# Optimization experiments

Measured on AMD Instinct MI355X. Metric: run time of the kernel, lower is better.

The kernel has to match this reference:

```python
import jax, jax.numpy as jnp
import numpy as np

STATE_LEN = 128
SEQ_LEN = 2048
NUM_ITERS = 2
DIM_IN = 1024
DIM_H = 64
BATCH = 2
T_TOTAL = SEQ_LEN + 2 * STATE_LEN  # 2304
NEG = -1e30  # large-negative causal mask (avoids -inf NaNs under autodiff)


def _ln(x, g, b):
    m = jnp.mean(x, axis=-1, keepdims=True)
    v = jnp.var(x, axis=-1, keepdims=True)
    return (x - m) / jnp.sqrt(v + 1e-5) * g + b


def setup_inputs() -> dict:
    key = jax.random.key(0)
    ks = jax.random.split(key, 16)

    def w(k, fi, fo):
        # torch nn.Linear-style fan-in scaled init (keeps logits O(1))
        return jax.random.normal(k, (fi, fo), jnp.float32) / np.sqrt(fi)

    return {
        "x": jax.random.normal(ks[0], (BATCH, T_TOTAL, DIM_IN), jnp.float32),
        "Wh": w(ks[1], DIM_IN, DIM_H),
        "Whs": w(ks[2], DIM_IN, DIM_H),
        "Whe": w(ks[3], DIM_IN, DIM_H),
        "Wk": w(ks[4], DIM_H, DIM_H),
        "Wq": w(ks[5], DIM_H, DIM_H),
        "Wv": w(ks[6], DIM_H, DIM_H),
        "Wks": w(ks[7], DIM_H, DIM_H),
        "Wqs": w(ks[8], DIM_H, DIM_H),
        "Wvs": w(ks[9], DIM_H, DIM_H),
        "Wke": w(ks[10], DIM_H, DIM_H),
        "Wqe": w(ks[11], DIM_H, DIM_H),
        "Wve": w(ks[12], DIM_H, DIM_H),
        "ln_g": jnp.ones((DIM_IN,), jnp.float32),
        "ln_b": jnp.zeros((DIM_IN,), jnp.float32),
        "ln_gs": jnp.ones((DIM_IN,), jnp.float32),
        "ln_bs": jnp.zeros((DIM_IN,), jnp.float32),
        "ln_ge": jnp.ones((DIM_IN,), jnp.float32),
        "ln_be": jnp.zeros((DIM_IN,), jnp.float32),
        "cope_emb": jax.random.normal(ks[13], (DIM_H, T_TOTAL), jnp.float32),
    }


def reference(x, Wh, Whs, Whe, Wk, Wq, Wv, Wks, Wqs, Wvs, Wke, Wqe, Wve,
              ln_g, ln_b, ln_gs, ln_bs, ln_ge, ln_be, cope_emb):
    S = STATE_LEN
    # extract_state: [state_start | seq | state_end] along token dim
    xs, xm, xe = x[:, :S], x[:, S:-S], x[:, -S:]
    xm = _ln(xm, ln_g, ln_b)
    xs = _ln(xs, ln_gs, ln_bs)
    xe = _ln(xe, ln_ge, ln_be)

    mem = xm @ Wh                 # (B, L, D)
    mem_s = xs @ Whs              # (B, S, D)
    mem_e = xe @ Whe              # (B, S, D)

    scale = 1.0 / np.sqrt(DIM_H)  # xformers default scale (beta=None)
    tril = jnp.tril(jnp.ones((T_TOTAL, T_TOTAL), bool))
    mask = jnp.where(tril, 0.0, NEG)  # log of lower-triangular ones

    mem_full = None
    for ix in range(NUM_ITERS):
        k = jnp.concatenate([mem_s @ Wks, mem @ Wk, mem_e @ Wke], axis=1)  # (B,T,D)
        q = jnp.concatenate([mem_s @ Wqs, mem @ Wq, mem_e @ Wqe], axis=1)
        v = jnp.concatenate([mem_s @ Wvs, mem @ Wv, mem_e @ Wve], axis=1)

        logits = jnp.einsum('btd,bsd->bts', q, k)  # unscaled, as in CoPE gates
        if ix == 0:
            # CoPE: sigmoid-gated reverse cumsum positions + interpolated embedding bias
            gates = jax.nn.sigmoid(logits)
            pos = jnp.flip(jnp.cumsum(jnp.flip(gates, -1), axis=-1), -1)
            pos = jnp.minimum(pos, float(T_TOTAL - 1))
            pos_floor = jnp.floor(pos)
            pos_ceil = jnp.ceil(pos)
            logits_int = jnp.einsum('btd,dn->btn', q, cope_emb)  # (B,T,T)
            lc = jnp.take_along_axis(logits_int, pos_ceil.astype(jnp.int32), axis=-1)
            lf = jnp.take_along_axis(logits_int, pos_floor.astype(jnp.int32), axis=-1)
            wfrac = pos - pos_floor
            bias = lc * wfrac + lf * (1.0 - wfrac)
            scores = logits * scale + mask + bias
        else:
            scores = logits * scale + mask

        attn = jax.nn.softmax(scores, axis=-1)
        mem_full = jnp.einsum('bts,bsd->btd', attn, v)  # (B,T,D)
        if ix < NUM_ITERS - 1:
            mem_s, mem, mem_e = mem_full[:, :S], mem_full[:, S:-S], mem_full[:, -S:]
    return mem_full
```

## Files before the change

### kernel.cpp

```cpp
#include <hip/hip_runtime.h>

#define T_TOT 2304
#define S_LEN 128
#define D_IN  1024
#define D_H   64
#define BATCH 2
#define NROW  (BATCH * T_TOT)
#define CH    (T_TOT / 256)
#define SCALE 0.125f
#define KCHUNKS 8
#define KCW   (D_IN / KCHUNKS)
#define TB    16
#define FCH   288
#define NSC   8
#define NTBLK (T_TOT / TB)

typedef unsigned short u16;
typedef __attribute__((ext_vector_type(8))) short short8;
typedef __attribute__((ext_vector_type(4))) float f32x4;
typedef __attribute__((ext_vector_type(4))) unsigned short u16x4;

static __device__ __forceinline__ u16 f2bf(float f) {
    unsigned u = __float_as_uint(f);
    unsigned r = (u + 0x7fffu + ((u >> 16) & 1u)) >> 16;
    return (u16)r;
}
static __device__ __forceinline__ float bf2f(u16 s) {
    return __uint_as_float((unsigned)s << 16);
}

__global__ __launch_bounds__(256) void k_ln(
    const float* __restrict__ x,
    const float* __restrict__ ln_g,  const float* __restrict__ ln_b,
    const float* __restrict__ ln_gs, const float* __restrict__ ln_bs,
    const float* __restrict__ ln_ge, const float* __restrict__ ln_be,
    u16* __restrict__ xn_hi, u16* __restrict__ xn_lo)
{
    __shared__ float red1[256], red2[256];
    const int row = blockIdx.x;
    const int t = row % T_TOT;
    const int tid = threadIdx.x;

    const float *gg, *bb;
    if (t < S_LEN)               { gg = ln_gs; bb = ln_bs; }
    else if (t >= T_TOT - S_LEN) { gg = ln_ge; bb = ln_be; }
    else                         { gg = ln_g;  bb = ln_b;  }

    const float4 xv = *(const float4*)(x + (size_t)row * D_IN + 4 * tid);
    float s  = xv.x + xv.y + xv.z + xv.w;
    float s2 = xv.x * xv.x + xv.y * xv.y + xv.z * xv.z + xv.w * xv.w;
    red1[tid] = s; red2[tid] = s2; __syncthreads();
    for (int off = 128; off > 0; off >>= 1) {
        if (tid < off) { red1[tid] += red1[tid + off]; red2[tid] += red2[tid + off]; }
        __syncthreads();
    }
    const float mean = red1[0] * (1.f / D_IN);
    const float var  = red2[0] * (1.f / D_IN) - mean * mean;
    const float rstd = rsqrtf(var + 1e-5f);

    const float4 gv = *(const float4*)(gg + 4 * tid);
    const float4 bv = *(const float4*)(bb + 4 * tid);
    float o0 = (xv.x - mean) * rstd * gv.x + bv.x;
    float o1 = (xv.y - mean) * rstd * gv.y + bv.y;
    float o2 = (xv.z - mean) * rstd * gv.z + bv.z;
    float o3 = (xv.w - mean) * rstd * gv.w + bv.w;

    u16x4 hv, lv;
    hv[0] = f2bf(o0); lv[0] = f2bf(o0 - bf2f(hv[0]));
    hv[1] = f2bf(o1); lv[1] = f2bf(o1 - bf2f(hv[1]));
    hv[2] = f2bf(o2); lv[2] = f2bf(o2 - bf2f(hv[2]));
    hv[3] = f2bf(o3); lv[3] = f2bf(o3 - bf2f(hv[3]));
    *(u16x4*)(xn_hi + (size_t)row * D_IN + 4 * tid) = hv;
    *(u16x4*)(xn_lo + (size_t)row * D_IN + 4 * tid) = lv;
}

#define WPREP_N (3 * D_H * D_IN)
__global__ __launch_bounds__(256) void k_prep(
    const float* __restrict__ Wh, const float* __restrict__ Whs, const float* __restrict__ Whe,
    const float* __restrict__ cope,
    u16* __restrict__ wT_hi, u16* __restrict__ wT_lo,
    u16* __restrict__ cT_hi, u16* __restrict__ cT_lo)
{
    const int gid = blockIdx.x * 256 + threadIdx.x;
    if (gid < WPREP_N) {
        const int seg = gid >> 16;
        const int o = gid & 65535;
        const int j = o >> 10, k = o & 1023;
        const float* W = seg == 0 ? Wh : (seg == 1 ? Whs : Whe);
        const float f = W[k * D_H + j];
        const u16 hi = f2bf(f);
        wT_hi[gid] = hi;
        wT_lo[gid] = f2bf(f - bf2f(hi));
    } else {
        const int idx = gid - WPREP_N;
        if (idx < T_TOT * D_H) {
            const int n = idx >> 6, d = idx & 63;
            const float f = cope[(size_t)d * T_TOT + n];
            const u16 hi = f2bf(f);
            cT_hi[idx] = hi;
            cT_lo[idx] = f2bf(f - bf2f(hi));
        }
    }
}

__global__ __launch_bounds__(256) void k_hgemm(
    const u16* __restrict__ xn_hi, const u16* __restrict__ xn_lo,
    const u16* __restrict__ wT_hi, const u16* __restrict__ wT_lo,
    float* __restrict__ h_part)
{
    const int tile = blockIdx.x;
    const int kc   = blockIdx.y;
    const int k0   = kc * KCW;
    const int tt = tile % 36;
    const int seg = tt < 2 ? 1 : (tt >= 34 ? 2 : 0);

    __shared__ u16 Bh[64 * KCW];
    __shared__ u16 Bl[64 * KCW];

    const int tid = threadIdx.x;
    {
        const int r = tid >> 2;
        const int c0 = (tid & 3) * 32;
        const u16* sh = wT_hi + ((size_t)seg * D_H + r) * D_IN + k0 + c0;
        const u16* sl = wT_lo + ((size_t)seg * D_H + r) * D_IN + k0 + c0;
        const int sw = (r & 7) << 3;
        #pragma unroll
        for (int u = 0; u < 4; ++u) {
            const int col = c0 + 8 * u;
            *(short8*)&Bh[r * KCW + (col ^ sw)] = *(const short8*)(sh + 8 * u);
            *(short8*)&Bl[r * KCW + (col ^ sw)] = *(const short8*)(sl + 8 * u);
        }
    }
    __syncthreads();

    const int w = tid >> 6;
    const int lane = tid & 63;
    const int l15 = lane & 15, lg4 = lane >> 4;
    const int row0 = tile * 64 + w * 16;

    const size_t abase = (size_t)(row0 + l15) * D_IN + k0 + 8 * lg4;
    f32x4 acc[4] = {};

    #pragma unroll
    for (int kk = 0; kk < KCW / 32; ++kk) {
        short8 ah = *(const short8*)(xn_hi + abase + kk * 32);
        short8 al = *(const short8*)(xn_lo + abase + kk * 32);
        #pragma unroll
        for (int j = 0; j < 4; ++j) {
            const int brow = j * 16 + l15;
            const int col = (kk * 32 + 8 * lg4) ^ ((brow & 7) << 3);
            short8 bh = *(const short8*)&Bh[brow * KCW + col];
            short8 bl = *(const short8*)&Bl[brow * KCW + col];
            acc[j] = __builtin_amdgcn_mfma_f32_16x16x32_bf16(al, bh, acc[j], 0, 0, 0);
            acc[j] = __builtin_amdgcn_mfma_f32_16x16x32_bf16(ah, bl, acc[j], 0, 0, 0);
            acc[j] = __builtin_amdgcn_mfma_f32_16x16x32_bf16(ah, bh, acc[j], 0, 0, 0);
        }
    }
    float* hp = h_part + (size_t)kc * ((size_t)NROW * D_H);
    #pragma unroll
    for (int j = 0; j < 4; ++j)
        #pragma unroll
        for (int r = 0; r < 4; ++r)
            hp[(size_t)(row0 + 4 * lg4 + r) * D_H + j * 16 + l15] = acc[j][r];
}

__global__ __launch_bounds__(256) void k_hred(
    const float* __restrict__ h_part, float* __restrict__ h)
{
    const size_t idx = (size_t)blockIdx.x * 256 + threadIdx.x;
    const size_t N = (size_t)NROW * D_H;
    float s = 0.f;
    #pragma unroll
    for (int kc = 0; kc < KCHUNKS; ++kc) s += h_part[kc * N + idx];
    h[idx] = s;
}

template <bool SPLIT>
__global__ __launch_bounds__(192) void k_qkv(
    const float* __restrict__ hin,
    const float* __restrict__ Wk,  const float* __restrict__ Wq,  const float* __restrict__ Wv,
    const float* __restrict__ Wks, const float* __restrict__ Wqs, const float* __restrict__ Wvs,
    const float* __restrict__ Wke, const float* __restrict__ Wqe, const float* __restrict__ Wve,
    u16* __restrict__ q_hi, u16* __restrict__ q_lo,
    u16* __restrict__ k_hi, u16* __restrict__ k_lo,
    u16* __restrict__ vT)
{
    __shared__ float hr[D_H];
    const int bid = blockIdx.x;
    const int b = bid / T_TOT, t = bid % T_TOT;
    const int tid = threadIdx.x;

    const float* hrow = hin + ((size_t)b * T_TOT + t) * D_H;
    if (tid < D_H) hr[tid] = hrow[tid];
    __syncthreads();

    const int which = tid >> 6, j = tid & 63;
    const float* W;
    if (t < S_LEN)               W = which == 0 ? Wks : (which == 1 ? Wqs : Wvs);
    else if (t >= T_TOT - S_LEN) W = which == 0 ? Wke : (which == 1 ? Wqe : Wve);
    else                         W = which == 0 ? Wk  : (which == 1 ? Wq  : Wv);

    float acc = 0.f;
    #pragma unroll
    for (int d = 0; d < D_H; ++d) acc += hr[d] * W[d * D_H + j];

    const size_t idx = ((size_t)b * T_TOT + t) * D_H + j;
    u16 hi = f2bf(acc);
    if (which == 0) {
        k_hi[idx] = hi;
        if (SPLIT) k_lo[idx] = f2bf(acc - bf2f(hi));
    } else if (which == 1) {
        q_hi[idx] = hi;
        if (SPLIT) q_lo[idx] = f2bf(acc - bf2f(hi));
    } else {
        vT[((size_t)b * D_H + j) * T_TOT + t] = hi;
    }
}

__global__ __launch_bounds__(256) void k_score2(
    const u16* __restrict__ a_hi, const u16* __restrict__ a_lo,
    const u16* __restrict__ k_hi, const u16* __restrict__ k_lo,
    const u16* __restrict__ c_hi, const u16* __restrict__ c_lo,
    float* __restrict__ logits, float* __restrict__ lint)
{
    const int b  = blockIdx.z;
    const int s0 = blockIdx.x * 64;
    const int wid = threadIdx.x >> 6;
    const int t0 = blockIdx.y * 64 + wid * 16;
    const int lane = threadIdx.x & 63;
    const int l15 = lane & 15, lg4 = lane >> 4;

    const size_t a_off = ((size_t)(b * T_TOT + t0 + l15)) * D_H + 8 * lg4;
    const short8 ah0 = *(const short8*)(a_hi + a_off);
    const short8 ah1 = *(const short8*)(a_hi + a_off + 32);
    const short8 al0 = *(const short8*)(a_lo + a_off);
    const short8 al1 = *(const short8*)(a_lo + a_off + 32);

    const size_t orow_off = ((size_t)(b * T_TOT + t0 + 4 * lg4)) * T_TOT + s0 + l15;

    const u16* bh = k_hi + (size_t)b * (T_TOT * D_H);
    const u16* bl = k_lo + (size_t)b * (T_TOT * D_H);
    float* o = logits + orow_off;

    #pragma unroll
    for (int pass = 0; pass < 2; ++pass) {
        #pragma unroll
        for (int ni = 0; ni < 4; ++ni) {
            const size_t b_off = ((size_t)(s0 + ni * 16 + l15)) * D_H + 8 * lg4;
            short8 bh0 = *(const short8*)(bh + b_off);
            short8 bh1 = *(const short8*)(bh + b_off + 32);
            short8 bl0 = *(const short8*)(bl + b_off);
            short8 bl1 = *(const short8*)(bl + b_off + 32);
            f32x4 acc = {0.f, 0.f, 0.f, 0.f};
            acc = __builtin_amdgcn_mfma_f32_16x16x32_bf16(al0, bh0, acc, 0, 0, 0);
            acc = __builtin_amdgcn_mfma_f32_16x16x32_bf16(al1, bh1, acc, 0, 0, 0);
            acc = __builtin_amdgcn_mfma_f32_16x16x32_bf16(ah0, bl0, acc, 0, 0, 0);
            acc = __builtin_amdgcn_mfma_f32_16x16x32_bf16(ah1, bl1, acc, 0, 0, 0);
            acc = __builtin_amdgcn_mfma_f32_16x16x32_bf16(ah0, bh0, acc, 0, 0, 0);
            acc = __builtin_amdgcn_mfma_f32_16x16x32_bf16(ah1, bh1, acc, 0, 0, 0);
            #pragma unroll
            for (int r = 0; r < 4; ++r)
                o[(size_t)r * T_TOT + ni * 16] = acc[r];
        }
        bh = c_hi; bl = c_lo;
        o = lint + orow_off;
    }
}

__global__ __launch_bounds__(256) void k_erow(
    const float* __restrict__ logits,
    const float* __restrict__ lint,
    float* __restrict__ pbase)
{
    __shared__ float lg[T_TOT];
    __shared__ float extra[2 * T_TOT];
    __shared__ float wtot[4], wmax[4], wsum[4];

    const int row = blockIdx.x;
    const int t = row % T_TOT;
    const int tid = threadIdx.x;
    const int lane = tid & 63, wid = tid >> 6;
    const float* lrow = logits + (size_t)row * T_TOT;

    for (int r = 0; r < CH; ++r) { int s = tid + 256 * r; lg[s] = lrow[s]; }
    __syncthreads();

    {
        const int base = tid * CH;
        float gv[CH];
        float lsum = 0.f;
        #pragma unroll
        for (int u = 0; u < CH; ++u) {
            float g = 1.f / (1.f + expf(-lg[base + u]));
            gv[u] = g;
            lsum += g;
        }
        float cs = lsum;
        #pragma unroll
        for (int off = 1; off < 64; off <<= 1) {
            float n = __shfl_up(cs, off);
            if (lane >= off) cs += n;
        }
        if (lane == 63) wtot[wid] = cs;
        __syncthreads();
        float pre = 0.f, tot = 0.f;
        #pragma unroll
        for (int w = 0; w < 4; ++w) {
            float vv = wtot[w];
            tot += vv;
            if (w < wid) pre += vv;
        }
        float run = pre + cs - lsum;
        #pragma unroll
        for (int u = 0; u < CH; ++u) {
            float p = fminf(tot - run, (float)(T_TOT - 1));
            extra[base + u] = p;
            run += gv[u];
        }
        const float* lintrow = lint + (size_t)row * T_TOT;
        for (int r = 0; r < CH; ++r) { int s = tid + 256 * r; extra[T_TOT + s] = lintrow[s]; }
        __syncthreads();
    }

    float scv[CH];
    float mx = -3.4e38f;
    #pragma unroll
    for (int r = 0; r < CH; ++r) {
        int sidx = tid + 256 * r;
        float sc = -3.4e38f;
        if (sidx <= t) {
            sc = lg[sidx] * SCALE;
            float p = extra[sidx];
            float pf = floorf(p);
            int fi = (int)pf;
            int ci = (int)ceilf(p);
            float w = p - pf;
            sc += extra[T_TOT + ci] * w + extra[T_TOT + fi] * (1.f - w);
            mx = fmaxf(mx, sc);
        }
        scv[r] = sc;
    }
    #pragma unroll
    for (int off = 32; off > 0; off >>= 1) mx = fmaxf(mx, __shfl_xor(mx, off));
    if (lane == 0) wmax[wid] = mx;
    __syncthreads();
    mx = fmaxf(fmaxf(wmax[0], wmax[1]), fmaxf(wmax[2], wmax[3]));

    float pvv[CH];
    float psum = 0.f;
    #pragma unroll
    for (int r = 0; r < CH; ++r) {
        int sidx = tid + 256 * r;
        float pv = 0.f;
        if (sidx <= t) { pv = expf(scv[r] - mx); psum += pv; }
        pvv[r] = pv;
    }
    #pragma unroll
    for (int off = 32; off > 0; off >>= 1) psum += __shfl_xor(psum, off);
    if (lane == 0) wsum[wid] = psum;
    __syncthreads();
    const float inv = 1.f / (wsum[0] + wsum[1] + wsum[2] + wsum[3]);

    u16* prow = (u16*)(pbase + (size_t)row * T_TOT);
    #pragma unroll
    for (int r = 0; r < CH; ++r) {
        int sidx = tid + 256 * r;
        prow[sidx] = f2bf(pvv[r] * inv);
    }
}

__global__ __launch_bounds__(256) void k_pv(
    const float* __restrict__ pbuf, const u16* __restrict__ vT,
    float* __restrict__ opart)
{
    const int b  = blockIdx.z;
    const int scn = blockIdx.y;
    const int bx = blockIdx.x;
    const int t0 = bx * 16;
    const int sstart = scn * FCH;
    const int send = min(sstart + FCH, t0 + 16);
    if (sstart >= send) return;

    const int j0 = (threadIdx.x >> 6) * 16;
    const int lane = threadIdx.x & 63;
    const int l15 = lane & 15, lg4 = lane >> 4;

    const u16* pb = (const u16*)pbuf
        + ((size_t)(b * T_TOT + t0 + l15)) * (2 * (size_t)T_TOT) + 8 * lg4;
    const u16* vb = vT + ((size_t)(b * D_H + j0 + l15)) * T_TOT + 8 * lg4;

    f32x4 a0 = {}, a1 = {}, a2 = {}, a3 = {};
    int s = sstart;
    for (; s + 128 <= send; s += 128) {
        short8 p0 = *(const short8*)(pb + s);
        short8 v0 = *(const short8*)(vb + s);
        short8 p1 = *(const short8*)(pb + s + 32);
        short8 v1 = *(const short8*)(vb + s + 32);
        short8 p2 = *(const short8*)(pb + s + 64);
        short8 v2 = *(const short8*)(vb + s + 64);
        short8 p3 = *(const short8*)(pb + s + 96);
        short8 v3 = *(const short8*)(vb + s + 96);
        a0 = __builtin_amdgcn_mfma_f32_16x16x32_bf16(p0, v0, a0, 0, 0, 0);
        a1 = __builtin_amdgcn_mfma_f32_16x16x32_bf16(p1, v1, a1, 0, 0, 0);
        a2 = __builtin_amdgcn_mfma_f32_16x16x32_bf16(p2, v2, a2, 0, 0, 0);
        a3 = __builtin_amdgcn_mfma_f32_16x16x32_bf16(p3, v3, a3, 0, 0, 0);
    }
    for (; s < send; s += 32) {
        short8 p0 = *(const short8*)(pb + s);
        short8 v0 = *(const short8*)(vb + s);
        a0 = __builtin_amdgcn_mfma_f32_16x16x32_bf16(p0, v0, a0, 0, 0, 0);
    }
    f32x4 acc = (a0 + a1) + (a2 + a3);
    float* ob = opart + (((size_t)(b * NTBLK + bx)) * NSC + scn) * (TB * D_H)
              + (size_t)(4 * lg4) * D_H + j0 + l15;
    #pragma unroll
    for (int r = 0; r < 4; ++r) ob[(size_t)r * D_H] = acc[r];
}

__global__ __launch_bounds__(256) void k_pvmerge(
    const float* __restrict__ opart, float* __restrict__ outp)
{
    const int bid = blockIdx.x;
    const int b = bid / NTBLK, bx = bid % NTBLK;
    const int t0 = bx * 16, t_max = t0 + 15;
    const int tid = threadIdx.x;
    const int tl = tid >> 4, j4 = (tid & 15) * 4;

    float4 acc = {0.f, 0.f, 0.f, 0.f};
    for (int scn = 0; scn < NSC; ++scn) {
        if (scn * FCH <= t_max) {
            const float4 v = *(const float4*)&opart[
                (((size_t)(b * NTBLK + bx)) * NSC + scn) * (TB * D_H) + tl * D_H + j4];
            acc.x += v.x; acc.y += v.y; acc.z += v.z; acc.w += v.w;
        }
    }
    *(float4*)&outp[((size_t)(b * T_TOT + t0 + tl)) * D_H + j4] = acc;
}

__global__ __launch_bounds__(256) void k_fattn1s(
    const u16* __restrict__ q_hi, const u16* __restrict__ k_hi,
    const u16* __restrict__ vT,
    float* __restrict__ fM, float* __restrict__ fD, float* __restrict__ fO)
{
    __shared__ u16 pstage[4][TB][32];

    const int b   = blockIdx.z;
    const int scn = blockIdx.y;
    const int bx  = blockIdx.x;
    const int t0 = bx * TB;
    const int t_max = t0 + TB - 1;
    if (scn * FCH > t_max) return;

    const int tid = threadIdx.x;
    const int wid = tid >> 6;
    const int lane = tid & 63;
    const int l15 = lane & 15, lg4 = lane >> 4;

    const size_t a_off = ((size_t)(b * T_TOT + t0 + l15)) * D_H + 8 * lg4;
    const short8 ah0 = *(const short8*)(q_hi + a_off);
    const short8 ah1 = *(const short8*)(q_hi + a_off + 32);
    const u16* kh = k_hi + (size_t)b * (T_TOT * D_H);

    const int w_lo  = scn * FCH + wid * (FCH / 4);
    const int w_end = min(w_lo + FCH / 4, t_max + 1);

    float m[4]   = {-3.0e38f, -3.0e38f, -3.0e38f, -3.0e38f};
    float den[4] = {0.f, 0.f, 0.f, 0.f};
    f32x4 oacc[4] = {};

    for (int s32 = w_lo; s32 < w_end; s32 += 32) {
        f32x4 acc0 = {0.f, 0.f, 0.f, 0.f};
        f32x4 acc1 = {0.f, 0.f, 0.f, 0.f};
        const bool ir1 = (s32 + 16) < w_end;
        {
            const size_t b_off = ((size_t)(s32 + l15)) * D_H + 8 * lg4;
            short8 b0 = *(const short8*)(kh + b_off);
            short8 b1 = *(const short8*)(kh + b_off + 32);
            acc0 = __builtin_amdgcn_mfma_f32_16x16x32_bf16(ah0, b0, acc0, 0, 0, 0);
            acc0 = __builtin_amdgcn_mfma_f32_16x16x32_bf16(ah1, b1, acc0, 0, 0, 0);
        }
        if (ir1) {
            const size_t b_off = ((size_t)(s32 + 16 + l15)) * D_H + 8 * lg4;
            short8 b0 = *(const short8*)(kh + b_off);
            short8 b1 = *(const short8*)(kh + b_off + 32);
            acc1 = __builtin_amdgcn_mfma_f32_16x16x32_bf16(ah0, b0, acc1, 0, 0, 0);
            acc1 = __builtin_amdgcn_mfma_f32_16x16x32_bf16(ah1, b1, acc1, 0, 0, 0);
        }
        #pragma unroll
        for (int r = 0; r < 4; ++r) {
            const int tl = 4 * lg4 + r;
            const int c0 = s32 + l15, c1 = s32 + 16 + l15;
            const bool v0 = (c0 < w_end) && (c0 <= t0 + tl);
            const bool v1 = ir1 && (c1 < w_end) && (c1 <= t0 + tl);
            const float sc0 = acc0[r] * SCALE;
            const float sc1 = acc1[r] * SCALE;
            float tmx = fmaxf(v0 ? sc0 : -3.0e38f, v1 ? sc1 : -3.0e38f);
            tmx = fmaxf(tmx, __shfl_xor(tmx, 1));
            tmx = fmaxf(tmx, __shfl_xor(tmx, 2));
            tmx = fmaxf(tmx, __shfl_xor(tmx, 4));
            tmx = fmaxf(tmx, __shfl_xor(tmx, 8));
            const float mn = fmaxf(m[r], tmx);
            const float scl = __expf(m[r] - mn);
            m[r] = mn;
            const float p0 = v0 ? __expf(sc0 - mn) : 0.f;
            const float p1 = v1 ? __expf(sc1 - mn) : 0.f;
            float ps = p0 + p1;
            ps += __shfl_xor(ps, 1); ps += __shfl_xor(ps, 2);
            ps += __shfl_xor(ps, 4); ps += __shfl_xor(ps, 8);
            den[r] = den[r] * scl + ps;
            #pragma unroll
            for (int j = 0; j < 4; ++j) oacc[j][r] *= scl;
            pstage[wid][tl][l15] = f2bf(p0);
            pstage[wid][tl][16 + l15] = f2bf(p1);
        }
        const short8 pa = *(const short8*)&pstage[wid][l15][8 * lg4];
        #pragma unroll
        for (int j = 0; j < 4; ++j) {
            const size_t v_off = ((size_t)(b * D_H + j * 16 + l15)) * T_TOT + s32 + 8 * lg4;
            short8 bv = *(const short8*)(vT + v_off);
            oacc[j] = __builtin_amdgcn_mfma_f32_16x16x32_bf16(pa, bv, oacc[j], 0, 0, 0);
        }
    }

    const size_t pidx = ((size_t)(b * NTBLK + bx)) * (NSC * 4) + scn * 4 + wid;
    if (l15 == 0) {
        #pragma unroll
        for (int r = 0; r < 4; ++r) {
            fM[pidx * TB + 4 * lg4 + r] = m[r];
            fD[pidx * TB + 4 * lg4 + r] = den[r];
        }
    }
    #pragma unroll
    for (int j = 0; j < 4; ++j)
        #pragma unroll
        for (int r = 0; r < 4; ++r)
            fO[pidx * (TB * D_H) + (size_t)(4 * lg4 + r) * D_H + j * 16 + l15] = oacc[j][r];
}

__global__ __launch_bounds__(256) void k_fmerge(
    const float* __restrict__ fM, const float* __restrict__ fD,
    const float* __restrict__ fO, float* __restrict__ outp)
{
    const int bid = blockIdx.x;
    const int b = bid / NTBLK, bx = bid % NTBLK;
    const int t0 = bx * 16, t_max = t0 + 15;
    const int tid = threadIdx.x;
    const int tl = tid >> 4, j4 = (tid & 15) * 4;
    const size_t pb = (size_t)bid * (NSC * 4);

    float M = -3.0e38f;
    #pragma unroll
    for (int c = 0; c < NSC * 4; ++c)
        if ((c >> 2) * FCH <= t_max) M = fmaxf(M, fM[(pb + c) * TB + tl]);

    float D = 0.f;
    float4 O = {0.f, 0.f, 0.f, 0.f};
    for (int c = 0; c < NSC * 4; ++c) {
        if ((c >> 2) * FCH <= t_max) {
            const float w = __expf(fM[(pb + c) * TB + tl] - M);
            D += w * fD[(pb + c) * TB + tl];
            const float4 ov = *(const float4*)&fO[(pb + c) * (TB * D_H) + tl * D_H + j4];
            O.x += w * ov.x; O.y += w * ov.y; O.z += w * ov.z; O.w += w * ov.w;
        }
    }
    const float inv = 1.f / D;
    float4 res; res.x = O.x * inv; res.y = O.y * inv; res.z = O.z * inv; res.w = O.w * inv;
    *(float4*)&outp[((size_t)(b * T_TOT + t0 + tl)) * D_H + j4] = res;
}

extern "C" void kernel_launch(void* const* d_in, const int* in_sizes, int n_in,
                              void* d_out, int out_size, void* d_ws, size_t ws_size,
                              hipStream_t stream) {
    const float* x    = (const float*)d_in[0];
    const float* Wh   = (const float*)d_in[1];
    const float* Whs  = (const float*)d_in[2];
    const float* Whe  = (const float*)d_in[3];
    const float* Wk   = (const float*)d_in[4];
    const float* Wq   = (const float*)d_in[5];
    const float* Wv   = (const float*)d_in[6];
    const float* Wks  = (const float*)d_in[7];
    const float* Wqs  = (const float*)d_in[8];
    const float* Wvs  = (const float*)d_in[9];
    const float* Wke  = (const float*)d_in[10];
    const float* Wqe  = (const float*)d_in[11];
    const float* Wve  = (const float*)d_in[12];
    const float* ln_g  = (const float*)d_in[13];
    const float* ln_b  = (const float*)d_in[14];
    const float* ln_gs = (const float*)d_in[15];
    const float* ln_bs = (const float*)d_in[16];
    const float* ln_ge = (const float*)d_in[17];
    const float* ln_be = (const float*)d_in[18];
    const float* cope  = (const float*)d_in[19];

    float* out = (float*)d_out;

    const size_t N = (size_t)NROW * D_H;
    char* W = (char*)d_ws;
    u16* xn_hi  = (u16*)W;    W += (size_t)NROW * D_IN * 2;
    u16* xn_lo  = (u16*)W;    W += (size_t)NROW * D_IN * 2;
    u16* wT_hi  = (u16*)W;    W += (size_t)3 * D_H * D_IN * 2;
    u16* wT_lo  = (u16*)W;    W += (size_t)3 * D_H * D_IN * 2;
    float* h    = (float*)W;  W += N * 4;
    u16* q_hi   = (u16*)W;    W += N * 2;
    u16* q_lo   = (u16*)W;    W += N * 2;
    u16* k_hi   = (u16*)W;    W += N * 2;
    u16* k_lo   = (u16*)W;    W += N * 2;
    u16* vT     = (u16*)W;    W += N * 2;
    u16* cT_hi  = (u16*)W;    W += (size_t)T_TOT * D_H * 2;
    u16* cT_lo  = (u16*)W;    W += (size_t)T_TOT * D_H * 2;
    float* logits = (float*)W; W += (size_t)BATCH * T_TOT * T_TOT * 4;
    float* lint   = (float*)W; W += (size_t)BATCH * T_TOT * T_TOT * 4;
    float* mem1   = (float*)W; W += N * 4;
    float* opart  = (float*)W; W += (size_t)BATCH * NTBLK * NSC * TB * D_H * 4;
    float* fM     = (float*)W; W += (size_t)BATCH * NTBLK * NSC * 4 * TB * 4;
    float* fD     = (float*)W; W += (size_t)BATCH * NTBLK * NSC * 4 * TB * 4;
    float* fO     = (float*)W; W += (size_t)BATCH * NTBLK * NSC * 4 * TB * D_H * 4;

    float* h_part = lint;

    k_ln<<<NROW, 256, 0, stream>>>(x, ln_g, ln_b, ln_gs, ln_bs, ln_ge, ln_be,
                                   xn_hi, xn_lo);
    k_prep<<<(WPREP_N + T_TOT * D_H + 255) / 256, 256, 0, stream>>>(
        Wh, Whs, Whe, cope, wT_hi, wT_lo, cT_hi, cT_lo);
    k_hgemm<<<dim3(NROW / 64, KCHUNKS), 256, 0, stream>>>(xn_hi, xn_lo, wT_hi, wT_lo, h_part);
    k_hred<<<(int)(N / 256), 256, 0, stream>>>(h_part, h);

    k_qkv<true><<<NROW, 192, 0, stream>>>(h, Wk, Wq, Wv, Wks, Wqs, Wvs, Wke, Wqe, Wve,
                                          q_hi, q_lo, k_hi, k_lo, vT);
    k_score2<<<dim3(T_TOT / 64, T_TOT / 64, BATCH), 256, 0, stream>>>(
        q_hi, q_lo, k_hi, k_lo, cT_hi, cT_lo, logits, lint);
    k_erow<<<NROW, 256, 0, stream>>>(logits, lint, lint);
    k_pv<<<dim3(NTBLK, NSC, BATCH), 256, 0, stream>>>(lint, vT, opart);
    k_pvmerge<<<BATCH * NTBLK, 256, 0, stream>>>(opart, mem1);

    k_qkv<false><<<NROW, 192, 0, stream>>>(mem1, Wk, Wq, Wv, Wks, Wqs, Wvs, Wke, Wqe, Wve,
                                           q_hi, q_lo, k_hi, k_lo, vT);
    k_fattn1s<<<dim3(NTBLK, NSC, BATCH), 256, 0, stream>>>(q_hi, k_hi, vT, fM, fD, fO);
    k_fmerge<<<BATCH * NTBLK, 256, 0, stream>>>(fM, fD, fO, out);
}
```

Baseline: 182.1 us.

## Fuse per-16-column gate sums into score kernel and trim causal row traffic

The score kernel now computes sigmoid gate partial sums per 16-column tile and writes them out. A small new kernel reduces these into per-row gate totals. The row kernel uses each total to bound how much of the interpolation-logit row it loads and only loads causal logits. It also skips storing masked logits, uses nontemporal stores, and pads an LDS staging array to avoid bank conflicts. This cuts global memory reads and writes of the large T×T buffers, at the cost of an extra launch and an extra sigmoid per logit in the score kernel.

```diff
diff --git a/kernel.cpp b/kernel.cpp
--- a/kernel.cpp
+++ b/kernel.cpp
@@ -14,6 +14,8 @@
 #define FCH   288
 #define NSC   8
 #define NTBLK (T_TOT / TB)
+#define NT16  (T_TOT / 16)
+#define NPART (NSC * 4)
 
 typedef unsigned short u16;
 typedef __attribute__((ext_vector_type(8))) short short8;
@@ -217,16 +219,18 @@
     }
 }
 
-__global__ __launch_bounds__(256) void k_score2(
+__global__ __launch_bounds__(256) void k_score2c(
     const u16* __restrict__ a_hi, const u16* __restrict__ a_lo,
     const u16* __restrict__ k_hi, const u16* __restrict__ k_lo,
     const u16* __restrict__ c_hi, const u16* __restrict__ c_lo,
-    float* __restrict__ logits, float* __restrict__ lint)
+    float* __restrict__ logits, float* __restrict__ lint,
+    float* __restrict__ csum)
 {
     const int b  = blockIdx.z;
     const int s0 = blockIdx.x * 64;
     const int wid = threadIdx.x >> 6;
     const int t0 = blockIdx.y * 64 + wid * 16;
+    const int wt_max = t0 + 15;
     const int lane = threadIdx.x & 63;
     const int l15 = lane & 15, lg4 = lane >> 4;
 
@@ -238,12 +242,10 @@
 
     const size_t orow_off = ((size_t)(b * T_TOT + t0 + 4 * lg4)) * T_TOT + s0 + l15;
 
-    const u16* bh = k_hi + (size_t)b * (T_TOT * D_H);
-    const u16* bl = k_lo + (size_t)b * (T_TOT * D_H);
-    float* o = logits + orow_off;
-
-    #pragma unroll
-    for (int pass = 0; pass < 2; ++pass) {
+    {
+        const u16* bh = k_hi + (size_t)b * (T_TOT * D_H);
+        const u16* bl = k_lo + (size_t)b * (T_TOT * D_H);
+        float* o = logits + orow_off;
         #pragma unroll
         for (int ni = 0; ni < 4; ++ni) {
             const size_t b_off = ((size_t)(s0 + ni * 16 + l15)) * D_H + 8 * lg4;
@@ -258,18 +260,63 @@
             acc = __builtin_amdgcn_mfma_f32_16x16x32_bf16(ah1, bl1, acc, 0, 0, 0);
             acc = __builtin_amdgcn_mfma_f32_16x16x32_bf16(ah0, bh0, acc, 0, 0, 0);
             acc = __builtin_amdgcn_mfma_f32_16x16x32_bf16(ah1, bh1, acc, 0, 0, 0);
+            const int c16 = (s0 >> 4) + ni;
+            #pragma unroll
+            for (int r = 0; r < 4; ++r) {
+                float g = 1.f / (1.f + __expf(-acc[r]));
+                g += __shfl_xor(g, 1); g += __shfl_xor(g, 2);
+                g += __shfl_xor(g, 4); g += __shfl_xor(g, 8);
+                if (l15 == 0)
+                    csum[((size_t)(b * T_TOT + t0 + 4 * lg4 + r)) * NT16 + c16] = g;
+            }
+            if (s0 + ni * 16 <= wt_max) {
+                #pragma unroll
+                for (int r = 0; r < 4; ++r)
+                    __builtin_nontemporal_store(acc[r], &o[(size_t)r * T_TOT + ni * 16]);
+            }
+        }
+    }
+
+    {
+        float* o = lint + orow_off;
+        #pragma unroll
+        for (int ni = 0; ni < 4; ++ni) {
+            const size_t b_off = ((size_t)(s0 + ni * 16 + l15)) * D_H + 8 * lg4;
+            short8 bh0 = *(const short8*)(c_hi + b_off);
+            short8 bh1 = *(const short8*)(c_hi + b_off + 32);
+            short8 bl0 = *(const short8*)(c_lo + b_off);
+            short8 bl1 = *(const short8*)(c_lo + b_off + 32);
+            f32x4 acc = {0.f, 0.f, 0.f, 0.f};
+            acc = __builtin_amdgcn_mfma_f32_16x16x32_bf16(al0, bh0, acc, 0, 0, 0);
+            acc = __builtin_amdgcn_mfma_f32_16x16x32_bf16(al1, bh1, acc, 0, 0, 0);
+            acc = __builtin_amdgcn_mfma_f32_16x16x32_bf16(ah0, bl0, acc, 0, 0, 0);
+            acc = __builtin_amdgcn_mfma_f32_16x16x32_bf16(ah1, bl1, acc, 0, 0, 0);
+            acc = __builtin_amdgcn_mfma_f32_16x16x32_bf16(ah0, bh0, acc, 0, 0, 0);
+            acc = __builtin_amdgcn_mfma_f32_16x16x32_bf16(ah1, bh1, acc, 0, 0, 0);
             #pragma unroll
             for (int r = 0; r < 4; ++r)
-                o[(size_t)r * T_TOT + ni * 16] = acc[r];
-        }
-        bh = c_hi; bl = c_lo;
-        o = lint + orow_off;
-    }
+                __builtin_nontemporal_store(acc[r], &o[(size_t)r * T_TOT + ni * 16]);
+        }
+    }
+}
+
+__global__ __launch_bounds__(256) void k_csum(
+    const float* __restrict__ csum, float* __restrict__ totalv)
+{
+    const int row = blockIdx.x * 4 + (threadIdx.x >> 6);
+    const int lane = threadIdx.x & 63;
+    const size_t base = (size_t)row * NT16;
+    float v = csum[base + lane] + csum[base + 64 + lane];
+    if (128 + lane < NT16) v += csum[base + 128 + lane];
+    #pragma unroll
+    for (int off = 32; off > 0; off >>= 1) v += __shfl_xor(v, off);
+    if (lane == 0) totalv[row] = v;
 }
 
 __global__ __launch_bounds__(256) void k_erow(
     const float* __restrict__ logits,
     const float* __restrict__ lint,
+    const float* __restrict__ totalv,
     float* __restrict__ pbase)
 {
     __shared__ float lg[T_TOT];
@@ -278,11 +325,19 @@
 
     const int row = blockIdx.x;
     const int t = row % T_TOT;
+    const int Lt16 = (t | 15) + 1;
+    const int Lw = min((Lt16 + 31) & ~31, T_TOT);
     const int tid = threadIdx.x;
     const int lane = tid & 63, wid = tid >> 6;
     const float* lrow = logits + (size_t)row * T_TOT;
-
-    for (int r = 0; r < CH; ++r) { int s = tid + 256 * r; lg[s] = lrow[s]; }
+    const float tot = totalv[row];
+    const int Lc = min((int)tot + 2, T_TOT);
+
+    for (int s = tid; s < Lt16; s += 256) lg[s] = lrow[s];
+    {
+        const float* lintrow = lint + (size_t)row * T_TOT;
+        for (int s = tid; s < Lc; s += 256) extra[T_TOT + s] = lintrow[s];
+    }
     __syncthreads();
 
     {
@@ -291,7 +346,8 @@
         float lsum = 0.f;
         #pragma unroll
         for (int u = 0; u < CH; ++u) {
-            float g = 1.f / (1.f + expf(-lg[base + u]));
+            const int s = base + u;
+            float g = (s <= t) ? 1.f / (1.f + expf(-lg[s])) : 0.f;
             gv[u] = g;
             lsum += g;
         }
@@ -303,22 +359,22 @@
         }
         if (lane == 63) wtot[wid] = cs;
         __syncthreads();
-        float pre = 0.f, tot = 0.f;
+        float pre = 0.f;
         #pragma unroll
         for (int w = 0; w < 4; ++w) {
             float vv = wtot[w];
-            tot += vv;
             if (w < wid) pre += vv;
         }
         float run = pre + cs - lsum;
         #pragma unroll
         for (int u = 0; u < CH; ++u) {
-            float p = fminf(tot - run, (float)(T_TOT - 1));
-            extra[base + u] = p;
+            const int s = base + u;
+            if (s <= t) {
+                float p = fminf(fmaxf(tot - run, 0.f), (float)(T_TOT - 1));
+                extra[s] = p;
+            }
             run += gv[u];
         }
-        const float* lintrow = lint + (size_t)row * T_TOT;
-        for (int r = 0; r < CH; ++r) { int s = tid + 256 * r; extra[T_TOT + s] = lintrow[s]; }
         __syncthreads();
     }
 
@@ -365,7 +421,7 @@
     #pragma unroll
     for (int r = 0; r < CH; ++r) {
         int sidx = tid + 256 * r;
-        prow[sidx] = f2bf(pvv[r] * inv);
+        if (sidx < Lw) prow[sidx] = f2bf(pvv[r] * inv);
     }
 }
 
@@ -442,7 +498,7 @@
     const u16* __restrict__ vT,
     float* __restrict__ fM, float* __restrict__ fD, float* __restrict__ fO)
 {
-    __shared__ u16 pstage[4][TB][32];
+    __shared__ u16 pstage[4][TB][40];
 
     const int b   = blockIdx.z;
     const int scn = blockIdx.y;
@@ -522,7 +578,7 @@
         }
     }
 
-    const size_t pidx = ((size_t)(b * NTBLK + bx)) * (NSC * 4) + scn * 4 + wid;
+    const size_t pidx = ((size_t)(b * NTBLK + bx)) * NPART + scn * 4 + wid;
     if (l15 == 0) {
         #pragma unroll
         for (int r = 0; r < 4; ++r) {
@@ -546,16 +602,16 @@
     const int t0 = bx * 16, t_max = t0 + 15;
     const int tid = threadIdx.x;
     const int tl = tid >> 4, j4 = (tid & 15) * 4;
-    const size_t pb = (size_t)bid * (NSC * 4);
+    const size_t pb = (size_t)bid * NPART;
 
     float M = -3.0e38f;
     #pragma unroll
-    for (int c = 0; c < NSC * 4; ++c)
+    for (int c = 0; c < NPART; ++c)
         if ((c >> 2) * FCH <= t_max) M = fmaxf(M, fM[(pb + c) * TB + tl]);
 
     float D = 0.f;
     float4 O = {0.f, 0.f, 0.f, 0.f};
-    for (int c = 0; c < NSC * 4; ++c) {
+    for (int c = 0; c < NPART; ++c) {
         if ((c >> 2) * FCH <= t_max) {
             const float w = __expf(fM[(pb + c) * TB + tl] - M);
             D += w * fD[(pb + c) * TB + tl];
@@ -610,11 +666,13 @@
     u16* cT_lo  = (u16*)W;    W += (size_t)T_TOT * D_H * 2;
     float* logits = (float*)W; W += (size_t)BATCH * T_TOT * T_TOT * 4;
     float* lint   = (float*)W; W += (size_t)BATCH * T_TOT * T_TOT * 4;
+    float* csum   = (float*)W; W += (size_t)NROW * NT16 * 4;
+    float* totalv = (float*)W; W += (size_t)NROW * 4;
     float* mem1   = (float*)W; W += N * 4;
     float* opart  = (float*)W; W += (size_t)BATCH * NTBLK * NSC * TB * D_H * 4;
-    float* fM     = (float*)W; W += (size_t)BATCH * NTBLK * NSC * 4 * TB * 4;
-    float* fD     = (float*)W; W += (size_t)BATCH * NTBLK * NSC * 4 * TB * 4;
-    float* fO     = (float*)W; W += (size_t)BATCH * NTBLK * NSC * 4 * TB * D_H * 4;
+    float* fM     = (float*)W; W += (size_t)BATCH * NTBLK * NPART * TB * 4;
+    float* fD     = (float*)W; W += (size_t)BATCH * NTBLK * NPART * TB * 4;
+    float* fO     = (float*)W; W += (size_t)BATCH * NTBLK * NPART * TB * D_H * 4;
 
     float* h_part = lint;
 
@@ -627,9 +685,10 @@
 
     k_qkv<true><<<NROW, 192, 0, stream>>>(h, Wk, Wq, Wv, Wks, Wqs, Wvs, Wke, Wqe, Wve,
                                           q_hi, q_lo, k_hi, k_lo, vT);
-    k_score2<<<dim3(T_TOT / 64, T_TOT / 64, BATCH), 256, 0, stream>>>(
-        q_hi, q_lo, k_hi, k_lo, cT_hi, cT_lo, logits, lint);
-    k_erow<<<NROW, 256, 0, stream>>>(logits, lint, lint);
+    k_score2c<<<dim3(T_TOT / 64, T_TOT / 64, BATCH), 256, 0, stream>>>(
+        q_hi, q_lo, k_hi, k_lo, cT_hi, cT_lo, logits, lint, csum);
+    k_csum<<<NROW / 4, 256, 0, stream>>>(csum, totalv);
+    k_erow<<<NROW, 256, 0, stream>>>(logits, lint, totalv, lint);
     k_pv<<<dim3(NTBLK, NSC, BATCH), 256, 0, stream>>>(lint, vT, opart);
     k_pvmerge<<<BATCH * NTBLK, 256, 0, stream>>>(opart, mem1);
 
```

Measured after the change: 196.6 us. 1.08x slower.
